# Performance work log

Hardware: AMD Instinct MI355X
Metric: run time of the kernel (lower is better)

Reference implementation:

```python
import jax, jax.numpy as jnp
import numpy as np

B, IN_DIM, K, D = 8192, 1024, 2048, 256
TAU = 1.0
BN_EPS = 1e-5


def setup_inputs() -> dict:
    key = jax.random.key(0)
    ks = jax.random.split(key, 4)
    x = jax.random.normal(ks[0], (B, IN_DIM), dtype=jnp.float32)
    u = jax.random.uniform(ks[1], (B, K), dtype=jnp.float32)  # uniform for gumbel noise
    W = jax.random.normal(ks[2], (IN_DIM, D), dtype=jnp.float32) * 0.02
    b = jnp.zeros((D,), dtype=jnp.float32)
    gamma = jnp.ones((D,), dtype=jnp.float32)
    beta = jnp.zeros((D,), dtype=jnp.float32)
    E = jax.random.normal(ks[3], (K, D), dtype=jnp.float32)  # nn.Embedding default N(0,1)
    return {"x": x, "u": u, "W": W, "b": b, "gamma": gamma, "beta": beta, "E": E}


def reference(x, u, W, b, gamma, beta, E):
    # classifier + BatchNorm1d (training mode: batch stats, biased variance)
    h = x @ W + b                                   # [B, D]
    mu = jnp.mean(h, axis=0)
    var = jnp.var(h, axis=0)
    h = (h - mu) * jax.lax.rsqrt(var + BN_EPS) * gamma + beta
    # negative squared euclidean distance via ||h||^2 - 2 h.E^T + ||e||^2 (GEMM form,
    # avoids materializing [B, K, D])
    h2 = jnp.sum(h * h, axis=-1, keepdims=True)     # [B, 1]
    e2 = jnp.sum(E * E, axis=-1)                    # [K]
    logits = -(h2 - 2.0 * (h @ E.T) + e2)           # [B, K]
    # gumbel-softmax (soft) with tau
    g = -jnp.log(-jnp.log(u + 1e-10) + 1e-10)
    assignments = jax.nn.softmax((logits + g) / TAU, axis=-1)  # [B, K]
    z = assignments @ E                             # [B, D]
    probs = jax.nn.softmax(logits, axis=-1)
    return probs, z
```

## Files before the change

kernel.cpp:

```cpp
#include <hip/hip_runtime.h>
#include <math.h>

#define B_SZ 8192
#define IN_DIM 1024
#define K_CB 2048
#define D_SZ 256
#define BN_EPS 1e-5f

typedef _Float16 f16;
typedef _Float16 f16x8 __attribute__((ext_vector_type(8)));
typedef _Float16 f16x4 __attribute__((ext_vector_type(4)));
typedef float    f32x4 __attribute__((ext_vector_type(4)));

#define GLOAD_LDS16(g, l) __builtin_amdgcn_global_load_lds(                      \
    (const __attribute__((address_space(1))) unsigned int*)(g),                  \
    (__attribute__((address_space(3))) unsigned int*)(l), 16, 0, 0)

template<int BM, int BN, int BK, int EPI, bool A32>
__global__ __launch_bounds__(256) void gemm_mfma(
    const void* __restrict__ Aptr, int lda,
    const f16* __restrict__ Bptr, int ldb,
    void* __restrict__ Cptr, int ldc, int Kdim,
    const float* __restrict__ bias)
{
    constexpr int G    = BK / 8;
    constexpr int MASK = G - 1;
    constexpr int WM = BM / 2, WN = BN / 2;
    constexpr int FM = WM / 16, FN = WN / 16;
    constexpr int CH_A = BM * G;
    constexpr int CH_B = BN * G;

    __shared__ char lds[(BM + BN) * BK * 2];
    char* As = lds;
    char* Bs = lds + BM * BK * 2;

    const int tid  = threadIdx.x;
    const int w    = tid >> 6, lane = tid & 63;
    const int wm   = w >> 1,   wn   = w & 1;
    const int row0 = blockIdx.x * BM;
    const int col0 = blockIdx.y * BN;

    f32x4 acc[FM][FN] = {};

    for (int k0 = 0; k0 < Kdim; k0 += BK) {
        #pragma unroll
        for (int i = 0; i < CH_B / 256; ++i) {
            const int base = (i * 4 + w) * 64;
            const int s = base + lane;
            const int r = s / G, c = s % G;
            const f16* src = Bptr + (size_t)(col0 + r) * ldb + k0 + ((c ^ (r & MASK)) * 8);
            GLOAD_LDS16(src, Bs + base * 16);
        }
        if (!A32) {
            #pragma unroll
            for (int i = 0; i < CH_A / 256; ++i) {
                const int base = (i * 4 + w) * 64;
                const int s = base + lane;
                const int r = s / G, c = s % G;
                const f16* src = (const f16*)Aptr + (size_t)(row0 + r) * lda + k0 + ((c ^ (r & MASK)) * 8);
                GLOAD_LDS16(src, As + base * 16);
            }
        } else {
            #pragma unroll
            for (int i = 0; i < CH_A / 256; ++i) {
                const int s = i * 256 + tid;
                const int r = s / G, c = s % G;
                const float* src = (const float*)Aptr + (size_t)(row0 + r) * lda + k0 + c * 8;
                const float4 v0 = ((const float4*)src)[0];
                const float4 v1 = ((const float4*)src)[1];
                f16x8 d;
                d[0] = (f16)v0.x; d[1] = (f16)v0.y; d[2] = (f16)v0.z; d[3] = (f16)v0.w;
                d[4] = (f16)v1.x; d[5] = (f16)v1.y; d[6] = (f16)v1.z; d[7] = (f16)v1.w;
                *(f16x8*)(As + (r * G + (c ^ (r & MASK))) * 16) = d;
            }
        }
        __syncthreads();

        #pragma unroll
        for (int kk = 0; kk < BK / 32; ++kk) {
            f16x8 af[FM], bf[FN];
            #pragma unroll
            for (int m = 0; m < FM; ++m) {
                const int r = wm * WM + m * 16 + (lane & 15);
                const int g = (kk * 4 + (lane >> 4)) ^ (r & MASK);
                af[m] = *(const f16x8*)(As + r * (BK * 2) + g * 16);
            }
            #pragma unroll
            for (int n = 0; n < FN; ++n) {
                const int r = wn * WN + n * 16 + (lane & 15);
                const int g = (kk * 4 + (lane >> 4)) ^ (r & MASK);
                bf[n] = *(const f16x8*)(Bs + r * (BK * 2) + g * 16);
            }
            #pragma unroll
            for (int m = 0; m < FM; ++m)
                #pragma unroll
                for (int n = 0; n < FN; ++n)
                    acc[m][n] = __builtin_amdgcn_mfma_f32_16x16x32_f16(af[m], bf[n], acc[m][n], 0, 0, 0);
        }
        __syncthreads();
    }

    #pragma unroll
    for (int m = 0; m < FM; ++m) {
        const int rbase = row0 + wm * WM + m * 16 + (lane >> 4) * 4;
        #pragma unroll
        for (int n = 0; n < FN; ++n) {
            const int c = col0 + wn * WN + n * 16 + (lane & 15);
            #pragma unroll
            for (int j = 0; j < 4; ++j) {
                const float v = acc[m][n][j];
                if (EPI == 0) {
                    ((float*)Cptr)[(size_t)(rbase + j) * ldc + c] = v;
                } else {
                    ((f16*)Cptr)[(size_t)(rbase + j) * ldc + c] = (f16)(v + bias[c]);
                }
            }
        }
    }
}

__global__ __launch_bounds__(512, 2) void fused_sm(
    const f16* __restrict__ h16, const f16* __restrict__ E16,
    const float* __restrict__ e2v, const float* __restrict__ u,
    float* __restrict__ probs, f16* __restrict__ assign16)
{
    __shared__ f16 Bs[2][128 * 256];
    __shared__ float redA[8][16], redB[8][16], redC[8][16], redD[8][16];

    const int tid  = threadIdx.x;
    const int w    = tid >> 6, lane = tid & 63;
    const int q    = lane >> 4, r16 = lane & 15;
    const int row0 = blockIdx.x * 16;
    const int colL = w * 16 + r16;

    f16x8 af[8];
    {
        const f16* hrow = h16 + (size_t)(row0 + r16) * D_SZ + q * 8;
        #pragma unroll
        for (int kk = 0; kk < 8; ++kk) af[kk] = *(const f16x8*)(hrow + kk * 32);
    }

    f32x4 acc[16];
    #pragma unroll
    for (int n = 0; n < 16; ++n) acc[n] = (f32x4){0.f, 0.f, 0.f, 0.f};
    f16x4 gv[16];

    #pragma unroll
    for (int i = 0; i < 8; ++i) {
        const int base = (i * 8 + w) * 64;
        const int s = base + lane;
        const int r = s >> 5, cg = s & 31;
        GLOAD_LDS16(E16 + (size_t)r * D_SZ + ((cg ^ (r & 31)) * 8), (f16*)Bs[0] + base * 8);
    }
    __syncthreads();

    #pragma unroll
    for (int c = 0; c < 16; ++c) {
        const int buf = c & 1;
        if (c < 15) {
            #pragma unroll
            for (int i = 0; i < 8; ++i) {
                const int base = (i * 8 + w) * 64;
                const int s = base + lane;
                const int r = s >> 5, cg = s & 31;
                GLOAD_LDS16(E16 + (size_t)((c + 1) * 128 + r) * D_SZ + ((cg ^ (r & 31)) * 8),
                            (f16*)Bs[buf ^ 1] + base * 8);
            }
        }
        {
            const int col = c * 128 + colL;
            const float* up = u + (size_t)(row0 + q * 4) * K_CB + col;
            #pragma unroll
            for (int j = 0; j < 4; ++j) {
                const float uu = up[(size_t)j * K_CB];
                gv[c][j] = (f16)(-__logf(-__logf(uu + 1e-10f) + 1e-10f));
            }
        }
        #pragma unroll
        for (int kk = 0; kk < 8; ++kk) {
            const int gb = (kk * 4 + q) ^ (colL & 31);
            const f16x8 bf = *(const f16x8*)((const f16*)Bs[buf] + colL * 256 + gb * 8);
            acc[c] = __builtin_amdgcn_mfma_f32_16x16x32_f16(af[kk], bf, acc[c], 0, 0, 0);
        }
        __syncthreads();
    }

    float m1[4] = {-1e30f, -1e30f, -1e30f, -1e30f};
    float m2[4] = {-1e30f, -1e30f, -1e30f, -1e30f};
    #pragma unroll
    for (int n = 0; n < 16; ++n) {
        const float ec = e2v[n * 128 + colL];
        #pragma unroll
        for (int j = 0; j < 4; ++j) {
            const float lv = 2.f * acc[n][j] - ec;
            acc[n][j] = lv;
            m1[j] = fmaxf(m1[j], lv);
            m2[j] = fmaxf(m2[j], lv + (float)gv[n][j]);
        }
    }
    #pragma unroll
    for (int off = 1; off < 16; off <<= 1)
        #pragma unroll
        for (int j = 0; j < 4; ++j) {
            m1[j] = fmaxf(m1[j], __shfl_xor(m1[j], off));
            m2[j] = fmaxf(m2[j], __shfl_xor(m2[j], off));
        }
    if (r16 == 0)
        #pragma unroll
        for (int j = 0; j < 4; ++j) { redA[w][q * 4 + j] = m1[j]; redB[w][q * 4 + j] = m2[j]; }
    __syncthreads();
    #pragma unroll
    for (int j = 0; j < 4; ++j) {
        float a0 = fmaxf(redA[0][q * 4 + j], redA[1][q * 4 + j]);
        float a1 = fmaxf(redA[2][q * 4 + j], redA[3][q * 4 + j]);
        float a2 = fmaxf(redA[4][q * 4 + j], redA[5][q * 4 + j]);
        float a3 = fmaxf(redA[6][q * 4 + j], redA[7][q * 4 + j]);
        m1[j] = fmaxf(fmaxf(a0, a1), fmaxf(a2, a3));
        float b0 = fmaxf(redB[0][q * 4 + j], redB[1][q * 4 + j]);
        float b1 = fmaxf(redB[2][q * 4 + j], redB[3][q * 4 + j]);
        float b2 = fmaxf(redB[4][q * 4 + j], redB[5][q * 4 + j]);
        float b3 = fmaxf(redB[6][q * 4 + j], redB[7][q * 4 + j]);
        m2[j] = fmaxf(fmaxf(b0, b1), fmaxf(b2, b3));
    }

    float s1[4] = {0.f, 0.f, 0.f, 0.f}, s2[4] = {0.f, 0.f, 0.f, 0.f};
    #pragma unroll
    for (int n = 0; n < 16; ++n)
        #pragma unroll
        for (int j = 0; j < 4; ++j) {
            const float lv = acc[n][j];
            const float e1 = __expf(lv - m1[j]);
            const float eg = __expf(lv + (float)gv[n][j] - m2[j]);
            acc[n][j] = e1; gv[n][j] = (f16)eg;
            s1[j] += e1; s2[j] += eg;
        }
    #pragma unroll
    for (int off = 1; off < 16; off <<= 1)
        #pragma unroll
        for (int j = 0; j < 4; ++j) {
            s1[j] += __shfl_xor(s1[j], off);
            s2[j] += __shfl_xor(s2[j], off);
        }
    if (r16 == 0)
        #pragma unroll
        for (int j = 0; j < 4; ++j) { redC[w][q * 4 + j] = s1[j]; redD[w][q * 4 + j] = s2[j]; }
    __syncthreads();
    float r1[4], r2[4];
    #pragma unroll
    for (int j = 0; j < 4; ++j) {
        r1[j] = 1.f / (redC[0][q * 4 + j] + redC[1][q * 4 + j] + redC[2][q * 4 + j] +
                       redC[3][q * 4 + j] + redC[4][q * 4 + j] + redC[5][q * 4 + j] +
                       redC[6][q * 4 + j] + redC[7][q * 4 + j]);
        r2[j] = 1.f / (redD[0][q * 4 + j] + redD[1][q * 4 + j] + redD[2][q * 4 + j] +
                       redD[3][q * 4 + j] + redD[4][q * 4 + j] + redD[5][q * 4 + j] +
                       redD[6][q * 4 + j] + redD[7][q * 4 + j]);
    }

    #pragma unroll
    for (int n = 0; n < 16; ++n) {
        const int col = n * 128 + colL;
        #pragma unroll
        for (int j = 0; j < 4; ++j) {
            const int row = row0 + q * 4 + j;
            probs[(size_t)row * K_CB + col] = acc[n][j] * r1[j];
            assign16[(size_t)row * K_CB + col] = (f16)((float)gv[n][j] * r2[j]);
        }
    }
}

__global__ __launch_bounds__(256) void conv_WT(const float* __restrict__ W, f16* __restrict__ WT)
{
    const int r = blockIdx.x, c = threadIdx.x;
    WT[c * 1024 + r] = (f16)W[r * 256 + c];
}

__global__ __launch_bounds__(256) void conv_E2(const float* __restrict__ E,
                                               f16* __restrict__ E16, f16* __restrict__ ET,
                                               float* __restrict__ e2)
{
    const int r = blockIdx.x, c = threadIdx.x;
    const int wave = c >> 6, lane = c & 63;
    const float v = E[r * 256 + c];
    E16[r * 256 + c] = (f16)v;
    ET[c * 2048 + r] = (f16)v;
    float ss = v * v;
    #pragma unroll
    for (int off = 32; off > 0; off >>= 1) ss += __shfl_down(ss, off);
    __shared__ float s4[4];
    if (lane == 0) s4[wave] = ss;
    __syncthreads();
    if (c == 0) e2[r] = s4[0] + s4[1] + s4[2] + s4[3];
}

__global__ __launch_bounds__(256) void bn_partial(const f16* __restrict__ h16, float* __restrict__ part)
{
    const int d = threadIdx.x;
    const int blk = blockIdx.x;
    const int r0 = blk * (B_SZ / 128);
    float s = 0.f, sq = 0.f;
    for (int r = r0; r < r0 + (B_SZ / 128); ++r) {
        const float v = (float)h16[(size_t)r * D_SZ + d];
        s += v; sq += v * v;
    }
    part[blk * 512 + d]       = s;
    part[blk * 512 + 256 + d] = sq;
}

__global__ __launch_bounds__(256) void bn_finalize(
    const float* __restrict__ part, const float* __restrict__ gamma, const float* __restrict__ beta,
    float* __restrict__ scale, float* __restrict__ shift)
{
    const int d = threadIdx.x;
    float s = 0.f, sq = 0.f;
    for (int b = 0; b < 128; ++b) { s += part[b * 512 + d]; sq += part[b * 512 + 256 + d]; }
    const float mu  = s / (float)B_SZ;
    const float var = sq / (float)B_SZ - mu * mu;
    const float sc  = gamma[d] * rsqrtf(var + BN_EPS);
    scale[d] = sc;
    shift[d] = beta[d] - mu * sc;
}

__global__ __launch_bounds__(256) void norm_h(
    f16* __restrict__ h16, const float* __restrict__ scale, const float* __restrict__ shift)
{
    const int wave = threadIdx.x >> 6, lane = threadIdx.x & 63;
    const int row = blockIdx.x * 4 + wave;
    f16x4* hp = (f16x4*)(h16 + (size_t)row * D_SZ);
    f16x4 v = hp[lane];
    const float4 sc = ((const float4*)scale)[lane];
    const float4 sh = ((const float4*)shift)[lane];
    v[0] = (f16)fmaf((float)v[0], sc.x, sh.x);
    v[1] = (f16)fmaf((float)v[1], sc.y, sh.y);
    v[2] = (f16)fmaf((float)v[2], sc.z, sh.z);
    v[3] = (f16)fmaf((float)v[3], sc.w, sh.w);
    hp[lane] = v;
}

extern "C" void kernel_launch(void* const* d_in, const int* in_sizes, int n_in,
                              void* d_out, int out_size, void* d_ws, size_t ws_size,
                              hipStream_t stream)
{
    const float* x     = (const float*)d_in[0];
    const float* u     = (const float*)d_in[1];
    const float* W     = (const float*)d_in[2];
    const float* bias  = (const float*)d_in[3];
    const float* gamma = (const float*)d_in[4];
    const float* beta  = (const float*)d_in[5];
    const float* E     = (const float*)d_in[6];

    float* probs = (float*)d_out;
    float* z     = probs + (size_t)B_SZ * K_CB;

    char* ws = (char*)d_ws;
    f16* assign16 = (f16*)ws;  ws += (size_t)B_SZ * K_CB * 2;
    f16* h16 = (f16*)ws;       ws += (size_t)B_SZ * D_SZ * 2;
    f16* WT16 = (f16*)ws;      ws += (size_t)D_SZ * IN_DIM * 2;
    f16* E16 = (f16*)ws;       ws += (size_t)K_CB * D_SZ * 2;
    f16* ET16 = (f16*)ws;      ws += (size_t)D_SZ * K_CB * 2;
    float* part = (float*)ws;  ws += 128 * 512 * 4;
    float* scale = (float*)ws; ws += D_SZ * 4;
    float* shift = (float*)ws; ws += D_SZ * 4;
    float* e2 = (float*)ws;    ws += K_CB * 4;

    conv_WT<<<IN_DIM, 256, 0, stream>>>(W, WT16);
    conv_E2<<<K_CB, 256, 0, stream>>>(E, E16, ET16, e2);

    {
        dim3 g(B_SZ / 64, D_SZ / 64);
        gemm_mfma<64, 64, 64, 1, true><<<g, 256, 0, stream>>>(
            x, IN_DIM, WT16, IN_DIM, h16, D_SZ, IN_DIM, bias);
    }
    bn_partial<<<128, 256, 0, stream>>>(h16, part);
    bn_finalize<<<1, 256, 0, stream>>>(part, gamma, beta, scale, shift);
    norm_h<<<B_SZ / 4, 256, 0, stream>>>(h16, scale, shift);

    fused_sm<<<B_SZ / 16, 512, 0, stream>>>(h16, E16, e2, u, probs, assign16);

    {
        dim3 g(B_SZ / 64, D_SZ / 64);
        gemm_mfma<64, 64, 128, 0, false><<<g, 256, 0, stream>>>(
            assign16, K_CB, ET16, K_CB, z, D_SZ, K_CB, nullptr);
    }
}
```

Measured before the change: 138.2 us.

## Double rows per block in fused softmax kernel and restructure E pipeline sync

Measured after the change: 196.6 us. 1.42x slower.

```diff
diff --git a/kernel.cpp b/kernel.cpp
--- a/kernel.cpp
+++ b/kernel.cpp
@@ -119,23 +119,26 @@
     }
 }
 
-__global__ __launch_bounds__(512, 2) void fused_sm(
+__global__ __launch_bounds__(1024, 4) void fused_sm(
     const f16* __restrict__ h16, const f16* __restrict__ E16,
     const float* __restrict__ e2v, const float* __restrict__ u,
     float* __restrict__ probs, f16* __restrict__ assign16)
 {
     __shared__ f16 Bs[2][128 * 256];
-    __shared__ float redA[8][16], redB[8][16], redC[8][16], redD[8][16];
+    __shared__ float redA[16][16], redB[16][16], redC[16][16], redD[16][16];
 
     const int tid  = threadIdx.x;
     const int w    = tid >> 6, lane = tid & 63;
     const int q    = lane >> 4, r16 = lane & 15;
-    const int row0 = blockIdx.x * 16;
-    const int colL = w * 16 + r16;
+    const int wg   = w >> 3;
+    const int wc   = w & 7;
+    const int row0 = blockIdx.x * 32;
+    const int rowA = row0 + wg * 16;
+    const int colL = wc * 16 + r16;
 
     f16x8 af[8];
     {
-        const f16* hrow = h16 + (size_t)(row0 + r16) * D_SZ + q * 8;
+        const f16* hrow = h16 + (size_t)(rowA + r16) * D_SZ + q * 8;
         #pragma unroll
         for (int kk = 0; kk < 8; ++kk) af[kk] = *(const f16x8*)(hrow + kk * 32);
     }
@@ -143,57 +146,57 @@
     f32x4 acc[16];
     #pragma unroll
     for (int n = 0; n < 16; ++n) acc[n] = (f32x4){0.f, 0.f, 0.f, 0.f};
-    f16x4 gv[16];
-
-    #pragma unroll
-    for (int i = 0; i < 8; ++i) {
-        const int base = (i * 8 + w) * 64;
+
+    #pragma unroll
+    for (int i = 0; i < 4; ++i) {
+        const int base = i * 1024 + w * 64;
         const int s = base + lane;
         const int r = s >> 5, cg = s & 31;
         GLOAD_LDS16(E16 + (size_t)r * D_SZ + ((cg ^ (r & 31)) * 8), (f16*)Bs[0] + base * 8);
     }
-    __syncthreads();
 
     #pragma unroll
     for (int c = 0; c < 16; ++c) {
         const int buf = c & 1;
         if (c < 15) {
             #pragma unroll
-            for (int i = 0; i < 8; ++i) {
-                const int base = (i * 8 + w) * 64;
+            for (int i = 0; i < 4; ++i) {
+                const int base = i * 1024 + w * 64;
                 const int s = base + lane;
                 const int r = s >> 5, cg = s & 31;
                 GLOAD_LDS16(E16 + (size_t)((c + 1) * 128 + r) * D_SZ + ((cg ^ (r & 31)) * 8),
                             (f16*)Bs[buf ^ 1] + base * 8);
             }
-        }
-        {
-            const int col = c * 128 + colL;
-            const float* up = u + (size_t)(row0 + q * 4) * K_CB + col;
-            #pragma unroll
-            for (int j = 0; j < 4; ++j) {
-                const float uu = up[(size_t)j * K_CB];
-                gv[c][j] = (f16)(-__logf(-__logf(uu + 1e-10f) + 1e-10f));
-            }
-        }
+            asm volatile("s_waitcnt vmcnt(4)" ::: "memory");
+        } else {
+            asm volatile("s_waitcnt vmcnt(0)" ::: "memory");
+        }
+        __builtin_amdgcn_s_barrier();
+        __builtin_amdgcn_sched_barrier(0);
         #pragma unroll
         for (int kk = 0; kk < 8; ++kk) {
             const int gb = (kk * 4 + q) ^ (colL & 31);
             const f16x8 bf = *(const f16x8*)((const f16*)Bs[buf] + colL * 256 + gb * 8);
             acc[c] = __builtin_amdgcn_mfma_f32_16x16x32_f16(af[kk], bf, acc[c], 0, 0, 0);
         }
-        __syncthreads();
+        __builtin_amdgcn_sched_barrier(0);
+        __builtin_amdgcn_s_barrier();
+        __builtin_amdgcn_sched_barrier(0);
     }
 
     float m1[4] = {-1e30f, -1e30f, -1e30f, -1e30f};
     float m2[4] = {-1e30f, -1e30f, -1e30f, -1e30f};
+    f16x4 gv[16];
     #pragma unroll
     for (int n = 0; n < 16; ++n) {
         const float ec = e2v[n * 128 + colL];
-        #pragma unroll
-        for (int j = 0; j < 4; ++j) {
+        const float* up = u + (size_t)(rowA + q * 4) * K_CB + n * 128 + colL;
+        #pragma unroll
+        for (int j = 0; j < 4; ++j) {
+            const float uu = up[(size_t)j * K_CB];
+            const float g = -__logf(-__logf(uu + 1e-10f) + 1e-10f);
+            gv[n][j] = (f16)g;
             const float lv = 2.f * acc[n][j] - ec;
-            acc[n][j] = lv;
             m1[j] = fmaxf(m1[j], lv);
             m2[j] = fmaxf(m2[j], lv + (float)gv[n][j]);
         }
@@ -211,29 +214,28 @@
     __syncthreads();
     #pragma unroll
     for (int j = 0; j < 4; ++j) {
-        float a0 = fmaxf(redA[0][q * 4 + j], redA[1][q * 4 + j]);
-        float a1 = fmaxf(redA[2][q * 4 + j], redA[3][q * 4 + j]);
-        float a2 = fmaxf(redA[4][q * 4 + j], redA[5][q * 4 + j]);
-        float a3 = fmaxf(redA[6][q * 4 + j], redA[7][q * 4 + j]);
-        m1[j] = fmaxf(fmaxf(a0, a1), fmaxf(a2, a3));
-        float b0 = fmaxf(redB[0][q * 4 + j], redB[1][q * 4 + j]);
-        float b1 = fmaxf(redB[2][q * 4 + j], redB[3][q * 4 + j]);
-        float b2 = fmaxf(redB[4][q * 4 + j], redB[5][q * 4 + j]);
-        float b3 = fmaxf(redB[6][q * 4 + j], redB[7][q * 4 + j]);
-        m2[j] = fmaxf(fmaxf(b0, b1), fmaxf(b2, b3));
+        float a = -1e30f, b = -1e30f;
+        #pragma unroll
+        for (int t = 0; t < 8; ++t) {
+            a = fmaxf(a, redA[wg * 8 + t][q * 4 + j]);
+            b = fmaxf(b, redB[wg * 8 + t][q * 4 + j]);
+        }
+        m1[j] = a; m2[j] = b;
     }
 
     float s1[4] = {0.f, 0.f, 0.f, 0.f}, s2[4] = {0.f, 0.f, 0.f, 0.f};
     #pragma unroll
-    for (int n = 0; n < 16; ++n)
-        #pragma unroll
-        for (int j = 0; j < 4; ++j) {
-            const float lv = acc[n][j];
-            const float e1 = __expf(lv - m1[j]);
-            const float eg = __expf(lv + (float)gv[n][j] - m2[j]);
-            acc[n][j] = e1; gv[n][j] = (f16)eg;
-            s1[j] += e1; s2[j] += eg;
-        }
+    for (int n = 0; n < 16; ++n) {
+        const float ec = e2v[n * 128 + colL];
+        #pragma unroll
+        for (int j = 0; j < 4; ++j) {
+            const float lv = 2.f * acc[n][j] - ec;
+            const float p1 = __expf(lv - m1[j]);
+            const float p2 = p1 * __expf((float)gv[n][j] + m1[j] - m2[j]);
+            acc[n][j] = p1; gv[n][j] = (f16)p2;
+            s1[j] += p1; s2[j] += p2;
+        }
+    }
     #pragma unroll
     for (int off = 1; off < 16; off <<= 1)
         #pragma unroll
@@ -248,12 +250,13 @@
     float r1[4], r2[4];
     #pragma unroll
     for (int j = 0; j < 4; ++j) {
-        r1[j] = 1.f / (redC[0][q * 4 + j] + redC[1][q * 4 + j] + redC[2][q * 4 + j] +
-                       redC[3][q * 4 + j] + redC[4][q * 4 + j] + redC[5][q * 4 + j] +
-                       redC[6][q * 4 + j] + redC[7][q * 4 + j]);
-        r2[j] = 1.f / (redD[0][q * 4 + j] + redD[1][q * 4 + j] + redD[2][q * 4 + j] +
-                       redD[3][q * 4 + j] + redD[4][q * 4 + j] + redD[5][q * 4 + j] +
-                       redD[6][q * 4 + j] + redD[7][q * 4 + j]);
+        float a = 0.f, b = 0.f;
+        #pragma unroll
+        for (int t = 0; t < 8; ++t) {
+            a += redC[wg * 8 + t][q * 4 + j];
+            b += redD[wg * 8 + t][q * 4 + j];
+        }
+        r1[j] = 1.f / a; r2[j] = 1.f / b;
     }
 
     #pragma unroll
@@ -261,7 +264,7 @@
         const int col = n * 128 + colL;
         #pragma unroll
         for (int j = 0; j < 4; ++j) {
-            const int row = row0 + q * 4 + j;
+            const int row = rowA + q * 4 + j;
             probs[(size_t)row * K_CB + col] = acc[n][j] * r1[j];
             assign16[(size_t)row * K_CB + col] = (f16)((float)gv[n][j] * r2[j]);
         }
@@ -374,7 +377,7 @@
     bn_finalize<<<1, 256, 0, stream>>>(part, gamma, beta, scale, shift);
     norm_h<<<B_SZ / 4, 256, 0, stream>>>(h16, scale, shift);
 
-    fused_sm<<<B_SZ / 16, 512, 0, stream>>>(h16, E16, e2, u, probs, assign16);
+    fused_sm<<<B_SZ / 32, 1024, 0, stream>>>(h16, E16, e2, u, probs, assign16);
 
     {
         dim3 g(B_SZ / 64, D_SZ / 64);
```
